# Kernel tuning notes

Measured on AMD Instinct MI355X. Metric: run time of the kernel, lower is better.

## Reference

```python
import jax, jax.numpy as jnp
import numpy as np

B, C, D, H, K = 512, 112, 128, 8, 8  # batch, channels(=seq), d_model, heads, conv kernel
HD = D // H
SCALE = HD ** -0.5
BN_EPS = 1e-5
LN_EPS = 1e-5


def setup_inputs() -> dict:
    key = jax.random.key(0)
    ks = jax.random.split(key, 12)
    s = 0.05
    return {
        "x": jax.random.normal(ks[0], (B, C, D), jnp.float32),
        "conv_w": jax.random.normal(ks[1], (C, 1, K), jnp.float32) * s,
        "conv_b": jax.random.normal(ks[2], (C,), jnp.float32) * s,
        "bn_g": jnp.ones((C,), jnp.float32),
        "bn_b": jnp.zeros((C,), jnp.float32),
        "bn_m": jnp.zeros((C,), jnp.float32),
        "bn_v": jnp.ones((C,), jnp.float32),
        "wq": jax.random.normal(ks[3], (D, D), jnp.float32) * s,
        "bq": jax.random.normal(ks[4], (D,), jnp.float32) * s,
        "wk": jax.random.normal(ks[5], (D, D), jnp.float32) * s,
        "bk": jax.random.normal(ks[6], (D,), jnp.float32) * s,
        "wv": jax.random.normal(ks[7], (D, D), jnp.float32) * s,
        "bv": jax.random.normal(ks[8], (D,), jnp.float32) * s,
        "wo": jax.random.normal(ks[9], (D, D), jnp.float32) * s,
        "bo": jax.random.normal(ks[10], (D,), jnp.float32) * s,
        "ln_g": jnp.ones((D,), jnp.float32),
        "ln_b": jnp.zeros((D,), jnp.float32),
    }


def _forward(x, conv_w, conv_b, bn_g, bn_b, bn_m, bn_v,
             wq, bq, wk, bk, wv, bv, wo, bo, ln_g, ln_b):
    # resnet_1: depthwise Conv1d(padding='same', k=8) -> GELU -> BatchNorm1d (eval)
    # torch 'same' padding for even k: left = (k-1)//2 = 3, right = 4
    h = jax.lax.conv_general_dilated(
        x, conv_w, window_strides=(1,), padding=[(3, 4)],
        dimension_numbers=("NCH", "OIH", "NCH"), feature_group_count=C)
    h = h + conv_b[None, :, None]
    h = jax.nn.gelu(h, approximate=False)
    h = (h - bn_m[None, :, None]) * (bn_g[None, :, None] * jax.lax.rsqrt(bn_v + BN_EPS)[None, :, None]) + bn_b[None, :, None]
    src = x + h  # [B, C, D]; attention treats C as sequence dim

    # multi-head attention (hand-rolled, res_attention path with prev=None)
    q = (src @ wq.T + bq).reshape(B, C, H, HD).transpose(0, 2, 1, 3)  # [B,H,S,hd]
    k = (src @ wk.T + bk).reshape(B, C, H, HD).transpose(0, 2, 1, 3)
    v = (src @ wv.T + bv).reshape(B, C, H, HD).transpose(0, 2, 1, 3)
    scores = jnp.einsum("bhqd,bhkd->bhqk", q, k) * SCALE  # [B,H,S,S]
    attn = jax.nn.softmax(scores, axis=-1)
    out = jnp.einsum("bhqk,bhkd->bhqd", attn, v)  # [B,H,S,hd]
    out = out.transpose(0, 2, 1, 3).reshape(B, C, D)
    out = out @ wo.T + bo

    # residual + LayerNorm over last dim
    src = src + out
    mu = jnp.mean(src, axis=-1, keepdims=True)
    var = jnp.mean(jnp.square(src - mu), axis=-1, keepdims=True)
    src = (src - mu) * jax.lax.rsqrt(var + LN_EPS) * ln_g + ln_b
    return src


def reference(x, conv_w, conv_b, bn_g, bn_b, bn_m, bn_v,
              wq, bq, wk, bk, wv, bv, wo, bo, ln_g, ln_b):
    return _forward(x, conv_w, conv_b, bn_g, bn_b, bn_m, bn_v,
                    wq, bq, wk, bk, wv, bv, wo, bo, ln_g, ln_b)
```

## Files before the change

kernel.cpp:

```cpp
#include <hip/hip_runtime.h>
#include <hip/hip_bf16.h>

#define BB 512
#define CC 112
#define DD 128
#define HH 8
#define HD 16
#define KK 8
#define SROW 140

typedef unsigned short u16;
typedef short short8 __attribute__((ext_vector_type(8)));
typedef float f32x4 __attribute__((ext_vector_type(4)));
typedef float f32x16 __attribute__((ext_vector_type(16)));

#define MFMA16(a, b, c) __builtin_amdgcn_mfma_f32_16x16x32_bf16(a, b, c, 0, 0, 0)
#define MFMA32(a, b, c) __builtin_amdgcn_mfma_f32_32x32x16_bf16(a, b, c, 0, 0, 0)

__device__ inline u16 f2bf(float f) {
  union { float f; unsigned u; } v{f};
  unsigned r = (v.u + 0x7FFFu + ((v.u >> 16) & 1u)) >> 16;
  return (u16)r;
}
__device__ inline float bf2f(u16 u) {
  union { unsigned u; float f; } v;
  v.u = ((unsigned)u) << 16;
  return v.f;
}
__device__ inline unsigned pk2(float a, float b) {
  __hip_bfloat162 h = __float22bfloat162_rn(float2{a, b});
  union { __hip_bfloat162 h; unsigned u; } v{h};
  return v.u;
}

__global__ __launch_bounds__(256) void k_wcvt(
    const float* __restrict__ wq, const float* __restrict__ wk,
    const float* __restrict__ wv, const float* __restrict__ wo,
    u16* __restrict__ w_b) {
  const int i = (blockIdx.x * 256 + threadIdx.x);
  const int sel = i >> 12, off = i & 4095;
  const float* w = (sel == 0) ? wq : (sel == 1) ? wk : (sel == 2) ? wv : wo;
  const float4 v = ((const float4*)w)[off];
  ((uint2*)w_b)[i] = uint2{pk2(v.x, v.y), pk2(v.z, v.w)};
}

__global__ __launch_bounds__(512, 4) void k_cqkv(
    const float* __restrict__ x, const float* __restrict__ cw,
    const float* __restrict__ cb, const float* __restrict__ bg,
    const float* __restrict__ bb_, const float* __restrict__ bm,
    const float* __restrict__ bv, const u16* __restrict__ w_b,
    const float* __restrict__ bq, const float* __restrict__ bk,
    const float* __restrict__ bvv,
    u16* __restrict__ src_b, u16* __restrict__ qb, u16* __restrict__ kb,
    u16* __restrict__ vtb) {
  __shared__ u16 S[CC * SROW];
  const int b = blockIdx.x;
  const int t = threadIdx.x;

  const int tg = t >> 2, sub = t & 3;
  if (tg < CC) {
    const int row = tg, ch = tg;
    const float4 w0 = *(const float4*)(cw + ch * KK);
    const float4 w1 = *(const float4*)(cw + ch * KK + 4);
    const float cbv = cb[ch];
    const float bscale = bg[ch] * rsqrtf(bv[ch] + 1e-5f);
    const float bmv = bm[ch], bbv = bb_[ch];
    const float* __restrict__ xr = x + ((size_t)b * CC + row) * DD;
    float in[40];
#pragma unroll
    for (int f = 0; f < 10; ++f) {
      const int fi = 8 * sub - 1 + f;
      float4 vv = {0.f, 0.f, 0.f, 0.f};
      if (fi >= 0 && fi < 32) vv = ((const float4*)xr)[fi];
      in[f * 4 + 0] = vv.x; in[f * 4 + 1] = vv.y;
      in[f * 4 + 2] = vv.z; in[f * 4 + 3] = vv.w;
    }
    unsigned pkv[16];
#pragma unroll
    for (int i2 = 0; i2 < 16; ++i2) {
      float oo[2];
#pragma unroll
      for (int j = 0; j < 2; ++j) {
        const int i = i2 * 2 + j;
        float a = 0.f;
        a = fmaf(in[i + 1], w0.x, a);
        a = fmaf(in[i + 2], w0.y, a);
        a = fmaf(in[i + 3], w0.z, a);
        a = fmaf(in[i + 4], w0.w, a);
        a = fmaf(in[i + 5], w1.x, a);
        a = fmaf(in[i + 6], w1.y, a);
        a = fmaf(in[i + 7], w1.z, a);
        a = fmaf(in[i + 8], w1.w, a);
        a += cbv;
        const float u = fmaf(0.044715f * a, a, 1.0f);
        const float e = __expf(a * u * -1.5957691216f);
        const float g = a * __frcp_rn(1.f + e);
        oo[j] = in[i + 4] + (g - bmv) * bscale + bbv;
      }
      pkv[i2] = pk2(oo[0], oo[1]);
    }
    u16* srow = S + row * SROW + sub * 32;
#pragma unroll
    for (int k2 = 0; k2 < 8; ++k2)
      *(uint2*)(srow + k2 * 4) = ((uint2*)pkv)[k2];
    uint4* gsr = (uint4*)(src_b + ((size_t)b * CC + row) * DD + sub * 32);
#pragma unroll
    for (int k4 = 0; k4 < 4; ++k4) gsr[k4] = ((uint4*)pkv)[k4];
  }
  __syncthreads();

  const int wave = t >> 6, lane = t & 63;
  const int quad = lane >> 4, n = lane & 15;
  const int h = wave;
  short8 Bf0[4], Bf1[4], Bf2[4];
#pragma unroll
  for (int kf = 0; kf < 4; ++kf) {
    const int wi = (h * 16 + n) * DD + kf * 32 + quad * 8;
    Bf0[kf] = *(const short8*)(w_b + wi);
    Bf1[kf] = *(const short8*)(w_b + 16384 + wi);
    Bf2[kf] = *(const short8*)(w_b + 32768 + wi);
  }
  const float bqv = bq[h * 16 + n];
  const float bkv = bk[h * 16 + n];
  const float bvv2 = bvv[h * 16 + n];
  u16* __restrict__ qhp = qb + (size_t)(b * HH + h) * CC * HD;
  u16* __restrict__ khp = kb + (size_t)(b * HH + h) * CC * HD;
  u16* __restrict__ vhp = vtb + (size_t)(b * HH + h) * HD * CC;
#pragma unroll
  for (int mt = 0; mt < 7; ++mt) {
    short8 A[4];
#pragma unroll
    for (int kf = 0; kf < 4; ++kf)
      A[kf] = *(const short8*)&S[(mt * 16 + n) * SROW + kf * 32 + quad * 8];
    f32x4 aq = {0.f, 0.f, 0.f, 0.f};
    f32x4 ak = {0.f, 0.f, 0.f, 0.f};
    f32x4 av = {0.f, 0.f, 0.f, 0.f};
#pragma unroll
    for (int kf = 0; kf < 4; ++kf) {
      aq = MFMA16(A[kf], Bf0[kf], aq);
      ak = MFMA16(A[kf], Bf1[kf], ak);
      av = MFMA16(A[kf], Bf2[kf], av);
    }
#pragma unroll
    for (int r = 0; r < 4; ++r) {
      const int row = mt * 16 + quad * 4 + r;
      qhp[row * HD + n] = f2bf(aq[r] + bqv);
      khp[row * HD + n] = f2bf(ak[r] + bkv);
      vhp[n * CC + row] = f2bf(av[r] + bvv2);
    }
  }
}

__global__ __launch_bounds__(512, 4) void k_attno(
    const u16* __restrict__ qb_, const u16* __restrict__ kb_,
    const u16* __restrict__ vtb_, const u16* __restrict__ w_bo,
    const float* __restrict__ bo, const u16* __restrict__ src_b,
    const float* __restrict__ lg, const float* __restrict__ lb,
    float* __restrict__ out) {
  __shared__ u16 AO[CC * SROW];
  const int b = blockIdx.x;
  const int t = threadIdx.x;
  const int wave = t >> 6, lane = t & 63;

  {
    const int h = wave;
    const int lo = lane & 31, hi = lane >> 5, hi8 = hi * 8;
    const u16* __restrict__ qh = qb_ + (size_t)(b * HH + h) * CC * HD;
    const u16* __restrict__ kh = kb_ + (size_t)(b * HH + h) * CC * HD;
    const u16* __restrict__ vth = vtb_ + (size_t)(b * HH + h) * HD * CC;
    for (int qt = 0; qt < 4; ++qt) {
      const int qt0 = qt * 32;
      short8 Bq = {};
      if (qt0 + lo < CC) Bq = *(const short8*)(qh + (qt0 + lo) * HD + hi8);
      f32x16 sa[4];
#pragma unroll
      for (int mt = 0; mt < 4; ++mt) {
        short8 Ak = {};
        const int key = mt * 32 + lo;
        if (key < CC) Ak = *(const short8*)(kh + key * HD + hi8);
        f32x16 z = {};
        sa[mt] = MFMA32(Ak, Bq, z);
      }
      const float C1 = 0.25f * 1.44269504088896341f;
      float mx = -1e30f;
#pragma unroll
      for (int mt = 0; mt < 4; ++mt) {
        const int rmax = (mt == 3) ? 8 : 16;
#pragma unroll
        for (int r = 0; r < 16; ++r)
          if (r < rmax) mx = fmaxf(mx, sa[mt][r]);
      }
      mx = fmaxf(mx, __shfl_xor(mx, 32));
      const float mxc = mx * C1;
      float sum = 0.f;
#pragma unroll
      for (int mt = 0; mt < 4; ++mt) {
        const int rmax = (mt == 3) ? 8 : 16;
#pragma unroll
        for (int r = 0; r < 16; ++r)
          if (r < rmax) {
            const float p = exp2f(fmaf(sa[mt][r], C1, -mxc));
            sa[mt][r] = p;
            sum += p;
          }
      }
      sum += __shfl_xor(sum, 32);
      const float rinv = 1.f / sum;
      unsigned U0[4][4], U1[4][4];
#pragma unroll
      for (int mt = 0; mt < 4; ++mt) {
        const int rqmax = (mt == 3) ? 2 : 4;
#pragma unroll
        for (int rq = 0; rq < 4; ++rq)
          if (rq < rqmax) {
            U0[mt][rq] =
                pk2(sa[mt][4 * rq + 0] * rinv, sa[mt][4 * rq + 1] * rinv);
            U1[mt][rq] =
                pk2(sa[mt][4 * rq + 2] * rinv, sa[mt][4 * rq + 3] * rinv);
          }
      }
      f32x16 oacc = {};
#pragma unroll
      for (int kt = 0; kt < 7; ++kt) {
        const int mt = kt >> 1;
        const int c = 2 * (kt & 1);
        const unsigned own0 = hi ? U0[mt][c + 1] : U0[mt][c];
        const unsigned own1 = hi ? U1[mt][c + 1] : U1[mt][c];
        const unsigned snd0 = hi ? U0[mt][c] : U0[mt][c + 1];
        const unsigned snd1 = hi ? U1[mt][c] : U1[mt][c + 1];
        const unsigned got0 = __shfl_xor(snd0, 32);
        const unsigned got1 = __shfl_xor(snd1, 32);
        union { unsigned u[4]; short8 s; } ap;
        ap.u[0] = hi ? got0 : own0;
        ap.u[1] = hi ? got1 : own1;
        ap.u[2] = hi ? own0 : got0;
        ap.u[3] = hi ? own1 : got1;
        short8 Bv = {};
        if (lo < HD) Bv = *(const short8*)(vth + lo * CC + kt * 16 + hi8);
        oacc = MFMA32(ap.s, Bv, oacc);
      }
      if (lo < HD) {
#pragma unroll
        for (int r = 0; r < 16; ++r) {
          const int qrow = qt0 + (r & 3) + 8 * (r >> 2) + 4 * hi;
          if (qrow < CC) AO[qrow * SROW + h * HD + lo] = f2bf(oacc[r]);
        }
      }
    }
  }
  __syncthreads();

  if (wave < 7) {
    const int quad = lane >> 4, n = lane & 15;
    const int mt = wave;
    short8 A[4];
#pragma unroll
    for (int kf = 0; kf < 4; ++kf)
      A[kf] = *(const short8*)&AO[(mt * 16 + n) * SROW + kf * 32 + quad * 8];
    float v[8][4];
#pragma unroll
    for (int nt = 0; nt < 8; ++nt) {
      f32x4 acc = {0.f, 0.f, 0.f, 0.f};
#pragma unroll
      for (int kf = 0; kf < 4; ++kf) {
        const short8 Bf =
            *(const short8*)(w_bo + (nt * 16 + n) * DD + kf * 32 + quad * 8);
        acc = MFMA16(A[kf], Bf, acc);
      }
      const int col = nt * 16 + n;
      const float bcol = bo[col];
#pragma unroll
      for (int r = 0; r < 4; ++r)
        v[nt][r] =
            acc[r] + bcol +
            bf2f(src_b[((size_t)b * CC + mt * 16 + quad * 4 + r) * DD + col]);
    }
    float sum[4] = {0.f, 0.f, 0.f, 0.f}, sq[4] = {0.f, 0.f, 0.f, 0.f};
#pragma unroll
    for (int nt = 0; nt < 8; ++nt)
#pragma unroll
      for (int r = 0; r < 4; ++r) {
        sum[r] += v[nt][r];
        sq[r] = fmaf(v[nt][r], v[nt][r], sq[r]);
      }
#pragma unroll
    for (int d = 1; d < 16; d <<= 1)
#pragma unroll
      for (int r = 0; r < 4; ++r) {
        sum[r] += __shfl_xor(sum[r], d);
        sq[r] += __shfl_xor(sq[r], d);
      }
    float mu[4], rs[4];
#pragma unroll
    for (int r = 0; r < 4; ++r) {
      mu[r] = sum[r] * (1.f / DD);
      const float var = sq[r] * (1.f / DD) - mu[r] * mu[r];
      rs[r] = rsqrtf(var + 1e-5f);
    }
#pragma unroll
    for (int nt = 0; nt < 8; ++nt) {
      const int col = nt * 16 + n;
      const float g = lg[col], be = lb[col];
#pragma unroll
      for (int r = 0; r < 4; ++r)
        out[((size_t)b * CC + mt * 16 + quad * 4 + r) * DD + col] =
            (v[nt][r] - mu[r]) * rs[r] * g + be;
    }
  }
}

extern "C" void kernel_launch(void* const* d_in, const int* in_sizes, int n_in,
                              void* d_out, int out_size, void* d_ws,
                              size_t ws_size, hipStream_t stream) {
  (void)in_sizes; (void)n_in; (void)out_size; (void)ws_size;
  const float* x   = (const float*)d_in[0];
  const float* cw  = (const float*)d_in[1];
  const float* cb  = (const float*)d_in[2];
  const float* bg  = (const float*)d_in[3];
  const float* bb  = (const float*)d_in[4];
  const float* bm  = (const float*)d_in[5];
  const float* bv  = (const float*)d_in[6];
  const float* wq  = (const float*)d_in[7];
  const float* bq  = (const float*)d_in[8];
  const float* wk  = (const float*)d_in[9];
  const float* bk  = (const float*)d_in[10];
  const float* wv  = (const float*)d_in[11];
  const float* bvv = (const float*)d_in[12];
  const float* wo  = (const float*)d_in[13];
  const float* bo  = (const float*)d_in[14];
  const float* lg  = (const float*)d_in[15];
  const float* lb  = (const float*)d_in[16];
  float* out = (float*)d_out;

  const size_t NE = (size_t)BB * CC * DD;
  u16* ub = (u16*)d_ws;
  u16* src_b = ub;
  u16* q_b   = ub + NE;
  u16* k_b   = ub + 2 * NE;
  u16* vt_b  = ub + 3 * NE;
  u16* w_b   = ub + 4 * NE;

  k_wcvt<<<64, 256, 0, stream>>>(wq, wk, wv, wo, w_b);
  k_cqkv<<<BB, 512, 0, stream>>>(x, cw, cb, bg, bb, bm, bv, w_b, bq, bk, bvv,
                                 src_b, q_b, k_b, vt_b);
  k_attno<<<BB, 512, 0, stream>>>(q_b, k_b, vt_b, w_b + 3 * 16384, bo, src_b,
                                  lg, lb, out);
}
```

Before: 174.0 us.

## Split attention blocks by query half, stage K/V in LDS, use permlane swaps

Doubles the attention+out-projection grid so each block handles half the query tiles (two 32-row tiles) of one batch, raising block-level parallelism. K and V for the batch are staged into LDS via direct global-to-LDS loads, since both halves and all query tiles reuse them. Cross-half shuffles use v_permlane32_swap instead of ds-based shuffles, and max/sum reductions use split accumulators for more ILP. The cost is loading K/V twice per batch, extra LDS use per block that may cut occupancy, and only 4 of 8 waves doing the output projection.

```diff
diff --git a/kernel.cpp b/kernel.cpp
--- a/kernel.cpp
+++ b/kernel.cpp
@@ -17,6 +17,11 @@
 #define MFMA16(a, b, c) __builtin_amdgcn_mfma_f32_16x16x32_bf16(a, b, c, 0, 0, 0)
 #define MFMA32(a, b, c) __builtin_amdgcn_mfma_f32_32x32x16_bf16(a, b, c, 0, 0, 0)
 
+#define GLD_LDS16(gsrc, ldst)                                          \
+  __builtin_amdgcn_global_load_lds(                                    \
+      (const __attribute__((address_space(1))) char*)(gsrc),           \
+      (__attribute__((address_space(3))) char*)(ldst), 16, 0, 0)
+
 __device__ inline u16 f2bf(float f) {
   union { float f; unsigned u; } v{f};
   unsigned r = (v.u + 0x7FFFu + ((v.u >> 16) & 1u)) >> 16;
@@ -31,6 +36,17 @@
   __hip_bfloat162 h = __float22bfloat162_rn(float2{a, b});
   union { __hip_bfloat162 h; unsigned u; } v{h};
   return v.u;
+}
+
+__device__ inline unsigned permx32(unsigned x) {
+  unsigned a = x, b = x;
+  asm("v_permlane32_swap_b32 %0, %1" : "+v"(a), "+v"(b));
+  return (threadIdx.x & 32) ? a : b;
+}
+__device__ inline float permx32f(float x) {
+  union { float f; unsigned u; } v{x};
+  v.u = permx32(v.u);
+  return v.f;
 }
 
 __global__ __launch_bounds__(256) void k_wcvt(
@@ -157,18 +173,39 @@
     const float* __restrict__ bo, const u16* __restrict__ src_b,
     const float* __restrict__ lg, const float* __restrict__ lb,
     float* __restrict__ out) {
-  __shared__ u16 AO[CC * SROW];
-  const int b = blockIdx.x;
+  __shared__ __attribute__((aligned(16))) u16 KL[HH * CC * HD];
+  __shared__ __attribute__((aligned(16))) u16 VL[HH * HD * CC];
+  __shared__ u16 AO[64 * SROW];
+  const int bid = blockIdx.x;
+  const int b = bid & (BB - 1);
+  const int hb = bid >> 9;
   const int t = threadIdx.x;
   const int wave = t >> 6, lane = t & 63;
+
+  {
+    const char* kg = (const char*)(kb_ + (size_t)b * (HH * CC * HD));
+    const char* vg = (const char*)(vtb_ + (size_t)b * (HH * HD * CC));
+    char* kl = (char*)KL;
+    char* vl = (char*)VL;
+#pragma unroll
+    for (int c0 = 0; c0 < 4; ++c0) {
+      const int c = wave + c0 * 8;
+      if (c < 28) {
+        GLD_LDS16(kg + c * 1024 + (lane << 4), kl + c * 1024);
+        GLD_LDS16(vg + c * 1024 + (lane << 4), vl + c * 1024);
+      }
+    }
+  }
+  __syncthreads();
 
   {
     const int h = wave;
     const int lo = lane & 31, hi = lane >> 5, hi8 = hi * 8;
     const u16* __restrict__ qh = qb_ + (size_t)(b * HH + h) * CC * HD;
-    const u16* __restrict__ kh = kb_ + (size_t)(b * HH + h) * CC * HD;
-    const u16* __restrict__ vth = vtb_ + (size_t)(b * HH + h) * HD * CC;
-    for (int qt = 0; qt < 4; ++qt) {
+    const u16* kh = KL + h * CC * HD;
+    const u16* vth = VL + h * HD * CC;
+    for (int qi = 0; qi < 2; ++qi) {
+      const int qt = 2 * hb + qi;
       const int qt0 = qt * 32;
       short8 Bq = {};
       if (qt0 + lo < CC) Bq = *(const short8*)(qh + (qt0 + lo) * HD + hi8);
@@ -182,17 +219,18 @@
         sa[mt] = MFMA32(Ak, Bq, z);
       }
       const float C1 = 0.25f * 1.44269504088896341f;
-      float mx = -1e30f;
+      float mxp[4] = {-1e30f, -1e30f, -1e30f, -1e30f};
 #pragma unroll
       for (int mt = 0; mt < 4; ++mt) {
         const int rmax = (mt == 3) ? 8 : 16;
 #pragma unroll
         for (int r = 0; r < 16; ++r)
-          if (r < rmax) mx = fmaxf(mx, sa[mt][r]);
-      }
-      mx = fmaxf(mx, __shfl_xor(mx, 32));
+          if (r < rmax) mxp[r & 3] = fmaxf(mxp[r & 3], sa[mt][r]);
+      }
+      float mx = fmaxf(fmaxf(mxp[0], mxp[1]), fmaxf(mxp[2], mxp[3]));
+      mx = fmaxf(mx, permx32f(mx));
       const float mxc = mx * C1;
-      float sum = 0.f;
+      float sp[4] = {0.f, 0.f, 0.f, 0.f};
 #pragma unroll
       for (int mt = 0; mt < 4; ++mt) {
         const int rmax = (mt == 3) ? 8 : 16;
@@ -201,10 +239,11 @@
           if (r < rmax) {
             const float p = exp2f(fmaf(sa[mt][r], C1, -mxc));
             sa[mt][r] = p;
-            sum += p;
+            sp[r & 3] += p;
           }
       }
-      sum += __shfl_xor(sum, 32);
+      float sum = (sp[0] + sp[1]) + (sp[2] + sp[3]);
+      sum += permx32f(sum);
       const float rinv = 1.f / sum;
       unsigned U0[4][4], U1[4][4];
 #pragma unroll
@@ -228,8 +267,8 @@
         const unsigned own1 = hi ? U1[mt][c + 1] : U1[mt][c];
         const unsigned snd0 = hi ? U0[mt][c] : U0[mt][c + 1];
         const unsigned snd1 = hi ? U1[mt][c] : U1[mt][c + 1];
-        const unsigned got0 = __shfl_xor(snd0, 32);
-        const unsigned got1 = __shfl_xor(snd1, 32);
+        const unsigned got0 = permx32(snd0);
+        const unsigned got1 = permx32(snd1);
         union { unsigned u[4]; short8 s; } ap;
         ap.u[0] = hi ? got0 : own0;
         ap.u[1] = hi ? got1 : own1;
@@ -242,69 +281,73 @@
       if (lo < HD) {
 #pragma unroll
         for (int r = 0; r < 16; ++r) {
-          const int qrow = qt0 + (r & 3) + 8 * (r >> 2) + 4 * hi;
-          if (qrow < CC) AO[qrow * SROW + h * HD + lo] = f2bf(oacc[r]);
+          const int rr = (r & 3) + 8 * (r >> 2) + 4 * hi;
+          if (qt0 + rr < CC)
+            AO[(qi * 32 + rr) * SROW + h * HD + lo] = f2bf(oacc[r]);
         }
       }
     }
   }
   __syncthreads();
 
-  if (wave < 7) {
-    const int quad = lane >> 4, n = lane & 15;
-    const int mt = wave;
-    short8 A[4];
-#pragma unroll
-    for (int kf = 0; kf < 4; ++kf)
-      A[kf] = *(const short8*)&AO[(mt * 16 + n) * SROW + kf * 32 + quad * 8];
-    float v[8][4];
-#pragma unroll
-    for (int nt = 0; nt < 8; ++nt) {
-      f32x4 acc = {0.f, 0.f, 0.f, 0.f};
-#pragma unroll
-      for (int kf = 0; kf < 4; ++kf) {
-        const short8 Bf =
-            *(const short8*)(w_bo + (nt * 16 + n) * DD + kf * 32 + quad * 8);
-        acc = MFMA16(A[kf], Bf, acc);
-      }
-      const int col = nt * 16 + n;
-      const float bcol = bo[col];
-#pragma unroll
-      for (int r = 0; r < 4; ++r)
-        v[nt][r] =
-            acc[r] + bcol +
-            bf2f(src_b[((size_t)b * CC + mt * 16 + quad * 4 + r) * DD + col]);
-    }
-    float sum[4] = {0.f, 0.f, 0.f, 0.f}, sq[4] = {0.f, 0.f, 0.f, 0.f};
-#pragma unroll
-    for (int nt = 0; nt < 8; ++nt)
+  if (wave < 4) {
+    const int mt = 4 * hb + wave;
+    if (mt < 7) {
+      const int quad = lane >> 4, n = lane & 15;
+      short8 A[4];
+#pragma unroll
+      for (int kf = 0; kf < 4; ++kf)
+        A[kf] =
+            *(const short8*)&AO[(wave * 16 + n) * SROW + kf * 32 + quad * 8];
+      float v[8][4];
+#pragma unroll
+      for (int nt = 0; nt < 8; ++nt) {
+        f32x4 acc = {0.f, 0.f, 0.f, 0.f};
+#pragma unroll
+        for (int kf = 0; kf < 4; ++kf) {
+          const short8 Bf =
+              *(const short8*)(w_bo + (nt * 16 + n) * DD + kf * 32 + quad * 8);
+          acc = MFMA16(A[kf], Bf, acc);
+        }
+        const int col = nt * 16 + n;
+        const float bcol = bo[col];
+#pragma unroll
+        for (int r = 0; r < 4; ++r)
+          v[nt][r] =
+              acc[r] + bcol +
+              bf2f(src_b[((size_t)b * CC + mt * 16 + quad * 4 + r) * DD + col]);
+      }
+      float sum[4] = {0.f, 0.f, 0.f, 0.f}, sq[4] = {0.f, 0.f, 0.f, 0.f};
+#pragma unroll
+      for (int nt = 0; nt < 8; ++nt)
+#pragma unroll
+        for (int r = 0; r < 4; ++r) {
+          sum[r] += v[nt][r];
+          sq[r] = fmaf(v[nt][r], v[nt][r], sq[r]);
+        }
+#pragma unroll
+      for (int d = 1; d < 16; d <<= 1)
+#pragma unroll
+        for (int r = 0; r < 4; ++r) {
+          sum[r] += __shfl_xor(sum[r], d);
+          sq[r] += __shfl_xor(sq[r], d);
+        }
+      float mu[4], rs[4];
 #pragma unroll
       for (int r = 0; r < 4; ++r) {
-        sum[r] += v[nt][r];
-        sq[r] = fmaf(v[nt][r], v[nt][r], sq[r]);
-      }
-#pragma unroll
-    for (int d = 1; d < 16; d <<= 1)
-#pragma unroll
-      for (int r = 0; r < 4; ++r) {
-        sum[r] += __shfl_xor(sum[r], d);
-        sq[r] += __shfl_xor(sq[r], d);
-      }
-    float mu[4], rs[4];
-#pragma unroll
-    for (int r = 0; r < 4; ++r) {
-      mu[r] = sum[r] * (1.f / DD);
-      const float var = sq[r] * (1.f / DD) - mu[r] * mu[r];
-      rs[r] = rsqrtf(var + 1e-5f);
-    }
-#pragma unroll
-    for (int nt = 0; nt < 8; ++nt) {
-      const int col = nt * 16 + n;
-      const float g = lg[col], be = lb[col];
-#pragma unroll
-      for (int r = 0; r < 4; ++r)
-        out[((size_t)b * CC + mt * 16 + quad * 4 + r) * DD + col] =
-            (v[nt][r] - mu[r]) * rs[r] * g + be;
+        mu[r] = sum[r] * (1.f / DD);
+        const float var = sq[r] * (1.f / DD) - mu[r] * mu[r];
+        rs[r] = rsqrtf(var + 1e-5f);
+      }
+#pragma unroll
+      for (int nt = 0; nt < 8; ++nt) {
+        const int col = nt * 16 + n;
+        const float g = lg[col], be = lb[col];
+#pragma unroll
+        for (int r = 0; r < 4; ++r)
+          out[((size_t)b * CC + mt * 16 + quad * 4 + r) * DD + col] =
+              (v[nt][r] - mu[r]) * rs[r] * g + be;
+      }
     }
   }
 }
@@ -343,6 +386,6 @@
   k_wcvt<<<64, 256, 0, stream>>>(wq, wk, wv, wo, w_b);
   k_cqkv<<<BB, 512, 0, stream>>>(x, cw, cb, bg, bb, bm, bv, w_b, bq, bk, bvv,
                                  src_b, q_b, k_b, vt_b);
-  k_attno<<<BB, 512, 0, stream>>>(q_b, k_b, vt_b, w_b + 3 * 16384, bo, src_b,
-                                  lg, lb, out);
-}
+  k_attno<<<2 * BB, 512, 0, stream>>>(q_b, k_b, vt_b, w_b + 3 * 16384, bo,
+                                      src_b, lg, lb, out);
+}
```

After: 172.3 us. About the same (-1.0%).
